# Optimization experiments

Measured on AMD Instinct MI355X. Metric: run time of the kernel, lower is better.

Reference implementation:

```python
import jax, jax.numpy as jnp
import numpy as np

M, K, N = 16, 8192, 8192
GROUP = 128


def setup_inputs() -> dict:
    key = jax.random.key(0)
    k1, k2, k3, k4 = jax.random.split(key, 4)
    x = jax.random.normal(k1, (M, K), dtype=jnp.float16)
    # packed INT4 weights: 8 nibbles per int32, row-major along K -> shape (K//8, N)
    qweight = jax.random.randint(k2, (K // 8, N), 0, 2147483647, dtype=jnp.int32)
    # per-group scales (K//GROUP, N); small positive values like real quant scales
    scales = (jax.random.uniform(k3, (K // GROUP, N), dtype=jnp.float16) * jnp.float16(0.01)
              + jnp.float16(0.001))
    bias = jax.random.normal(k4, (N,), dtype=jnp.float16) * jnp.float16(0.1)
    return {"x": x, "qweight": qweight, "scales": scales, "bias": bias}


def _dequant(qweight, scales):
    K8, n = qweight.shape
    shifts = jnp.arange(8, dtype=jnp.int32) * 4  # (8,)
    nib = (qweight[:, None, :] >> shifts[None, :, None]) & 0xF  # (K//8, 8, N)
    w = nib.reshape(K8 * 8, n).astype(scales.dtype) - jnp.asarray(8, scales.dtype)
    g = scales.shape[0]
    group = (K8 * 8) // g
    w = (w.reshape(g, group, n) * scales[:, None, :]).reshape(K8 * 8, n)
    return w  # (K, N) in scales dtype


def reference(x, qweight, scales, bias):
    # INT4 dequant (symmetric, zero-point 8) + GEMM + bias epilogue
    w = _dequant(qweight, scales)          # (K, N)
    out = jnp.dot(x, w) + bias             # (M, N)
    return out
```

## Files before the change

kernel.cpp:

```cpp
#include <hip/hip_runtime.h>


#define K_DIM 8192
#define N_DIM 8192

typedef _Float16 h2 __attribute__((ext_vector_type(2)));
typedef _Float16 h8 __attribute__((ext_vector_type(8)));
typedef float f32x4 __attribute__((ext_vector_type(4)));

union H8U { unsigned u[4]; h8 h; };

__device__ __forceinline__ unsigned pkrtz_u(float a, float b) {
  return __builtin_bit_cast(unsigned, __builtin_amdgcn_cvt_pkrtz(a, b));
}

__global__ __launch_bounds__(1024, 4) void qlin_kernel(
    const float* __restrict__ x,
    const int* __restrict__ qw,
    const float* __restrict__ scales,
    const float* __restrict__ bias,
    float* __restrict__ out) {
  __shared__ float red[16][512];

  const int tid = threadIdx.x;
  const int wave = tid >> 6;
  const int lane = tid & 63;
  const int c = lane & 15;
  const int quad = lane >> 4;
  const int nb = blockIdx.x * 32;

  f32x4 acc0 = {0.f, 0.f, 0.f, 0.f};
  f32x4 acc1 = {0.f, 0.f, 0.f, 0.f};

  const float* xp = x + (size_t)c * K_DIM + wave * 512 + quad * 8;
  const int* qp = qw + (size_t)(wave * 64 + quad) * N_DIM + nb + 2 * c;
  const float* sp = scales + (size_t)(wave * 4) * N_DIM + nb + 2 * c;

  const h2 koff = __builtin_bit_cast(h2, 0x64086408u);

#pragma unroll
  for (int g = 0; g < 4; ++g) {
    float2 sv = *(const float2*)sp;
    h2 s0 = __builtin_bit_cast(h2, pkrtz_u(sv.x, sv.x));
    h2 s1 = __builtin_bit_cast(h2, pkrtz_u(sv.y, sv.y));
#pragma unroll
    for (int it = 0; it < 4; ++it) {
      int2 q2 = *(const int2*)qp;
      float4 xa = *(const float4*)xp;
      float4 xb = *(const float4*)(xp + 4);
      H8U a, b0, b1;
      a.u[0] = pkrtz_u(xa.x, xb.x);
      a.u[1] = pkrtz_u(xa.y, xb.y);
      a.u[2] = pkrtz_u(xa.z, xb.z);
      a.u[3] = pkrtz_u(xa.w, xb.w);
      unsigned qa = (unsigned)q2.x, qb = (unsigned)q2.y;
#pragma unroll
      for (int p = 0; p < 4; ++p) {
        unsigned t0 = ((qa >> (4 * p)) & 0x000F000Fu) | 0x64006400u;
        unsigned t1 = ((qb >> (4 * p)) & 0x000F000Fu) | 0x64006400u;
        h2 w0 = (__builtin_bit_cast(h2, t0) - koff) * s0;
        h2 w1 = (__builtin_bit_cast(h2, t1) - koff) * s1;
        b0.u[p] = __builtin_bit_cast(unsigned, w0);
        b1.u[p] = __builtin_bit_cast(unsigned, w1);
      }
      acc0 = __builtin_amdgcn_mfma_f32_16x16x32_f16(a.h, b0.h, acc0, 0, 0, 0);
      acc1 = __builtin_amdgcn_mfma_f32_16x16x32_f16(a.h, b1.h, acc1, 0, 0, 0);
      qp += 4 * N_DIM;
      xp += 32;
    }
    sp += N_DIM;
  }

#pragma unroll
  for (int r = 0; r < 4; ++r) {
    int m = quad * 4 + r;
    red[wave][m * 32 + 2 * c] = acc0[r];
    red[wave][m * 32 + 2 * c + 1] = acc1[r];
  }
  __syncthreads();

  if (tid < 512) {
    int j = tid & 31;
    float v = 0.f;
#pragma unroll
    for (int w = 0; w < 16; ++w) v += red[w][tid];
    int n = nb + j;
    v += bias[n];
    out[(size_t)(tid >> 5) * N_DIM + n] = v;
  }
}

extern "C" void kernel_launch(void* const* d_in, const int* in_sizes, int n_in,
                              void* d_out, int out_size, void* d_ws, size_t ws_size,
                              hipStream_t stream) {
  const float* x      = (const float*)d_in[0];
  const int* qw       = (const int*)d_in[1];
  const float* scales = (const float*)d_in[2];
  const float* bias   = (const float*)d_in[3];
  float* out          = (float*)d_out;

  qlin_kernel<<<256, 1024, 0, stream>>>(x, qw, scales, bias, out);
}
```

Baseline: 93.00 us.

## Split-K with LDS-staged coalesced INT4 tiles and atomic accumulation

Replaces the one-block-per-32-columns kernel with a split-K grid of 512 blocks. Each block covers 256 columns by 512 K, stages packed INT4 weights into LDS with wide coalesced int4 loads, and reuses each activation fragment across four column tiles. Partial sums are reduced in LDS and then added to the output with float atomics. A separate kernel writes the bias into the output first. This aims to make weight loads coalesced and increase reuse, at the cost of an extra launch, atomic traffic, and non-deterministic summation order.

Result: slower. 94.92 us (+2.1%).

```diff
diff --git a/kernel.cpp b/kernel.cpp
--- a/kernel.cpp
+++ b/kernel.cpp
@@ -7,86 +7,109 @@
 typedef _Float16 h2 __attribute__((ext_vector_type(2)));
 typedef _Float16 h8 __attribute__((ext_vector_type(8)));
 typedef float f32x4 __attribute__((ext_vector_type(4)));
-
 union H8U { unsigned u[4]; h8 h; };
 
 __device__ __forceinline__ unsigned pkrtz_u(float a, float b) {
   return __builtin_bit_cast(unsigned, __builtin_amdgcn_cvt_pkrtz(a, b));
 }
 
-__global__ __launch_bounds__(1024, 4) void qlin_kernel(
+__global__ void bias_init_kernel(const float* __restrict__ bias, float* __restrict__ out) {
+  int i = blockIdx.x * 256 + threadIdx.x;
+  out[i] = bias[i & (N_DIM - 1)];
+}
+
+__global__ __launch_bounds__(512, 4) void qlin_main(
     const float* __restrict__ x,
     const int* __restrict__ qw,
     const float* __restrict__ scales,
-    const float* __restrict__ bias,
     float* __restrict__ out) {
-  __shared__ float red[16][512];
+  __shared__ int lds_q[16384];
 
   const int tid = threadIdx.x;
-  const int wave = tid >> 6;
-  const int lane = tid & 63;
-  const int c = lane & 15;
-  const int quad = lane >> 4;
-  const int nb = blockIdx.x * 32;
+  const int ntb = blockIdx.x & 31;
+  const int ksb = blockIdx.x >> 5;
+  const int nb = ntb << 8;
+  const int kb = ksb << 9;
+  const int rowbase = ksb << 6;
 
-  f32x4 acc0 = {0.f, 0.f, 0.f, 0.f};
-  f32x4 acc1 = {0.f, 0.f, 0.f, 0.f};
-
-  const float* xp = x + (size_t)c * K_DIM + wave * 512 + quad * 8;
-  const int* qp = qw + (size_t)(wave * 64 + quad) * N_DIM + nb + 2 * c;
-  const float* sp = scales + (size_t)(wave * 4) * N_DIM + nb + 2 * c;
-
-  const h2 koff = __builtin_bit_cast(h2, 0x64086408u);
-
+  const int* qg = qw + (size_t)rowbase * N_DIM + nb;
+  int4 v[8];
 #pragma unroll
-  for (int g = 0; g < 4; ++g) {
-    float2 sv = *(const float2*)sp;
-    h2 s0 = __builtin_bit_cast(h2, pkrtz_u(sv.x, sv.x));
-    h2 s1 = __builtin_bit_cast(h2, pkrtz_u(sv.y, sv.y));
+  for (int p = 0; p < 8; ++p) {
+    int idx = (p << 9) + tid;
+    int row = idx >> 6;
+    int c4 = (idx & 63) << 2;
+    v[p] = *(const int4*)(qg + (size_t)row * N_DIM + c4);
+  }
 #pragma unroll
-    for (int it = 0; it < 4; ++it) {
-      int2 q2 = *(const int2*)qp;
-      float4 xa = *(const float4*)xp;
-      float4 xb = *(const float4*)(xp + 4);
-      H8U a, b0, b1;
-      a.u[0] = pkrtz_u(xa.x, xb.x);
-      a.u[1] = pkrtz_u(xa.y, xb.y);
-      a.u[2] = pkrtz_u(xa.z, xb.z);
-      a.u[3] = pkrtz_u(xa.w, xb.w);
-      unsigned qa = (unsigned)q2.x, qb = (unsigned)q2.y;
-#pragma unroll
-      for (int p = 0; p < 4; ++p) {
-        unsigned t0 = ((qa >> (4 * p)) & 0x000F000Fu) | 0x64006400u;
-        unsigned t1 = ((qb >> (4 * p)) & 0x000F000Fu) | 0x64006400u;
-        h2 w0 = (__builtin_bit_cast(h2, t0) - koff) * s0;
-        h2 w1 = (__builtin_bit_cast(h2, t1) - koff) * s1;
-        b0.u[p] = __builtin_bit_cast(unsigned, w0);
-        b1.u[p] = __builtin_bit_cast(unsigned, w1);
-      }
-      acc0 = __builtin_amdgcn_mfma_f32_16x16x32_f16(a.h, b0.h, acc0, 0, 0, 0);
-      acc1 = __builtin_amdgcn_mfma_f32_16x16x32_f16(a.h, b1.h, acc1, 0, 0, 0);
-      qp += 4 * N_DIM;
-      xp += 32;
-    }
-    sp += N_DIM;
-  }
-
-#pragma unroll
-  for (int r = 0; r < 4; ++r) {
-    int m = quad * 4 + r;
-    red[wave][m * 32 + 2 * c] = acc0[r];
-    red[wave][m * 32 + 2 * c + 1] = acc1[r];
+  for (int p = 0; p < 8; ++p) {
+    int idx = (p << 9) + tid;
+    int row = idx >> 6;
+    int c4 = (idx & 63) << 2;
+    int L = (((row >> 2) << 4) + (c4 >> 4)) * 64 + ((row & 3) << 4) + (c4 & 15);
+    *(int4*)&lds_q[L] = v[p];
   }
   __syncthreads();
 
-  if (tid < 512) {
-    int j = tid & 31;
-    float v = 0.f;
+  const int wave = tid >> 6, lane = tid & 63;
+  const int wn = wave & 3, wk = wave >> 2;
+  const int c = lane & 15, q = lane >> 4;
+
+  h2 sc[2][4];
 #pragma unroll
-    for (int w = 0; w < 16; ++w) v += red[w][tid];
-    int n = nb + j;
-    v += bias[n];
-    out[(size_t)(tid >> 5) * N_DIM + n] = v;
+  for (int g2 = 0; g2 < 2; ++g2)
+#pragma unroll
+    for (int ct = 0; ct < 4; ++ct) {
+      float sv = scales[(size_t)((ksb << 2) + (wk << 1) + g2) * N_DIM +
+                        nb + (wn << 6) + (ct << 4) + c];
+      sc[g2][ct] = __builtin_bit_cast(h2, pkrtz_u(sv, sv));
+    }
+
+  const h2 koff = __builtin_bit_cast(h2, 0x64086408u);
+  f32x4 acc[4] = {{0.f,0.f,0.f,0.f},{0.f,0.f,0.f,0.f},{0.f,0.f,0.f,0.f},{0.f,0.f,0.f,0.f}};
+
+  const float* xp = x + (size_t)c * K_DIM + kb + (wk << 8) + (q << 3);
+#pragma unroll
+  for (int s = 0; s < 8; ++s) {
+    float4 xa = *(const float4*)xp;
+    float4 xb = *(const float4*)(xp + 4);
+    xp += 32;
+    H8U a;
+    a.u[0] = pkrtz_u(xa.x, xb.x);
+    a.u[1] = pkrtz_u(xa.y, xb.y);
+    a.u[2] = pkrtz_u(xa.z, xb.z);
+    a.u[3] = pkrtz_u(xa.w, xb.w);
+    int base = ((((wk << 3) + s) << 4) + (wn << 2)) * 64 + lane;
+#pragma unroll
+    for (int ct = 0; ct < 4; ++ct) {
+      unsigned qv = (unsigned)lds_q[base + (ct << 6)];
+      h2 s2 = sc[s >> 2][ct];
+      H8U b;
+#pragma unroll
+      for (int p = 0; p < 4; ++p) {
+        unsigned t = ((qv >> (4 * p)) & 0x000F000Fu) | 0x64006400u;
+        h2 w = (__builtin_bit_cast(h2, t) - koff) * s2;
+        b.u[p] = __builtin_bit_cast(unsigned, w);
+      }
+      acc[ct] = __builtin_amdgcn_mfma_f32_16x16x32_f16(a.h, b.h, acc[ct], 0, 0, 0);
+    }
+  }
+
+  __syncthreads();
+  float* red = (float*)lds_q;
+#pragma unroll
+  for (int ct = 0; ct < 4; ++ct)
+#pragma unroll
+    for (int r = 0; r < 4; ++r)
+      red[((wk << 4) + (q << 2) + r) * 256 + (wn << 6) + (ct << 4) + c] = acc[ct][r];
+  __syncthreads();
+
+#pragma unroll
+  for (int e = 0; e < 8; ++e) {
+    int idx = (e << 9) + tid;
+    int m = idx >> 8, j = idx & 255;
+    float vv = red[m * 256 + j] + red[(16 + m) * 256 + j];
+    unsafeAtomicAdd(&out[(size_t)m * N_DIM + nb + j], vv);
   }
 }
 
@@ -99,5 +122,6 @@
   const float* bias   = (const float*)d_in[3];
   float* out          = (float*)d_out;
 
-  qlin_kernel<<<256, 1024, 0, stream>>>(x, qw, scales, bias, out);
+  bias_init_kernel<<<512, 256, 0, stream>>>(bias, out);
+  qlin_main<<<512, 512, 0, stream>>>(x, qw, scales, out);
 }
```

## Split K across blocks with atomic reduction and prepack x to fp16

Applied to the files above, without the earlier changes.

The main kernel now splits K across four blocks per N tile (1024 blocks of 512 threads) and accumulates partial results into the output with atomic adds. The output is first initialised to the bias by a separate kernel. x is converted to packed fp16 MFMA layout once by a prepack kernel instead of in every block. All weight loads are issued up front and A-operand loads are double-buffered to expose more memory parallelism. The cost is two extra kernel launches, global atomics, and a non-deterministic summation order.

Result: faster. 86.12 us (-7.4%).

```diff
diff --git a/kernel.cpp b/kernel.cpp
--- a/kernel.cpp
+++ b/kernel.cpp
@@ -7,86 +7,107 @@
 typedef _Float16 h2 __attribute__((ext_vector_type(2)));
 typedef _Float16 h8 __attribute__((ext_vector_type(8)));
 typedef float f32x4 __attribute__((ext_vector_type(4)));
-
 union H8U { unsigned u[4]; h8 h; };
 
 __device__ __forceinline__ unsigned pkrtz_u(float a, float b) {
   return __builtin_bit_cast(unsigned, __builtin_amdgcn_cvt_pkrtz(a, b));
 }
+__device__ __forceinline__ h2 dup_h2(float v) {
+  return __builtin_bit_cast(h2, pkrtz_u(v, v));
+}
 
-__global__ __launch_bounds__(1024, 4) void qlin_kernel(
-    const float* __restrict__ x,
+__global__ void bias_init_kernel(const float* __restrict__ bias, float* __restrict__ out) {
+  int i = blockIdx.x * 256 + threadIdx.x;
+  out[i] = bias[i & (N_DIM - 1)];
+}
+
+__global__ void prepack_x_kernel(const float* __restrict__ x, unsigned* __restrict__ xpk) {
+  int S = blockIdx.x;
+  int L = threadIdx.x;
+  int q = L >> 4, m = L & 15;
+  const float* xp = x + (size_t)m * K_DIM + 32 * S + 8 * q;
+  float4 lo = *(const float4*)xp;
+  float4 hi = *(const float4*)(xp + 4);
+  unsigned* o = xpk + S * 256 + L * 4;
+  o[0] = pkrtz_u(lo.x, hi.x);
+  o[1] = pkrtz_u(lo.y, hi.y);
+  o[2] = pkrtz_u(lo.z, hi.z);
+  o[3] = pkrtz_u(lo.w, hi.w);
+}
+
+__global__ __launch_bounds__(512, 8) void qlin_main(
+    const unsigned* __restrict__ xpk,
     const int* __restrict__ qw,
     const float* __restrict__ scales,
-    const float* __restrict__ bias,
     float* __restrict__ out) {
-  __shared__ float red[16][512];
+  __shared__ float red[8][512];
 
   const int tid = threadIdx.x;
-  const int wave = tid >> 6;
+  const int wv = tid >> 6;
   const int lane = tid & 63;
   const int c = lane & 15;
   const int quad = lane >> 4;
-  const int nb = blockIdx.x * 32;
+  const int ntb = blockIdx.x & 255;
+  const int ksb = blockIdx.x >> 8;
+  const int nb = ntb * 32;
+  const int S0 = ksb * 64 + wv * 8;
+
+  const int* qp = qw + (size_t)(4 * S0 + quad) * N_DIM + nb + 2 * c;
+  int2 qv[8];
+#pragma unroll
+  for (int s = 0; s < 8; ++s) qv[s] = *(const int2*)(qp + (size_t)(4 * s) * N_DIM);
+  const float* sp = scales + (size_t)(S0 >> 2) * N_DIM + nb + 2 * c;
+  float2 svA = *(const float2*)sp;
+  float2 svB = *(const float2*)(sp + N_DIM);
+
+  const unsigned* ap = xpk + (size_t)S0 * 256 + lane * 4;
+  uint4 av[2];
+  av[0] = *(const uint4*)ap;
+
+  const h2 koff = __builtin_bit_cast(h2, 0x64086408u);
+  h2 s0A = dup_h2(svA.x), s1A = dup_h2(svA.y);
+  h2 s0B = dup_h2(svB.x), s1B = dup_h2(svB.y);
 
   f32x4 acc0 = {0.f, 0.f, 0.f, 0.f};
   f32x4 acc1 = {0.f, 0.f, 0.f, 0.f};
 
-  const float* xp = x + (size_t)c * K_DIM + wave * 512 + quad * 8;
-  const int* qp = qw + (size_t)(wave * 64 + quad) * N_DIM + nb + 2 * c;
-  const float* sp = scales + (size_t)(wave * 4) * N_DIM + nb + 2 * c;
-
-  const h2 koff = __builtin_bit_cast(h2, 0x64086408u);
-
 #pragma unroll
-  for (int g = 0; g < 4; ++g) {
-    float2 sv = *(const float2*)sp;
-    h2 s0 = __builtin_bit_cast(h2, pkrtz_u(sv.x, sv.x));
-    h2 s1 = __builtin_bit_cast(h2, pkrtz_u(sv.y, sv.y));
+  for (int s = 0; s < 8; ++s) {
+    if (s < 7) av[(s + 1) & 1] = *(const uint4*)(ap + (s + 1) * 256);
+    h2 s0 = (s < 4) ? s0A : s0B;
+    h2 s1 = (s < 4) ? s1A : s1B;
+    uint4 u = av[s & 1];
+    H8U a;
+    a.u[0] = u.x; a.u[1] = u.y; a.u[2] = u.z; a.u[3] = u.w;
+    unsigned qa = (unsigned)qv[s].x, qb = (unsigned)qv[s].y;
+    H8U b0, b1;
 #pragma unroll
-    for (int it = 0; it < 4; ++it) {
-      int2 q2 = *(const int2*)qp;
-      float4 xa = *(const float4*)xp;
-      float4 xb = *(const float4*)(xp + 4);
-      H8U a, b0, b1;
-      a.u[0] = pkrtz_u(xa.x, xb.x);
-      a.u[1] = pkrtz_u(xa.y, xb.y);
-      a.u[2] = pkrtz_u(xa.z, xb.z);
-      a.u[3] = pkrtz_u(xa.w, xb.w);
-      unsigned qa = (unsigned)q2.x, qb = (unsigned)q2.y;
-#pragma unroll
-      for (int p = 0; p < 4; ++p) {
-        unsigned t0 = ((qa >> (4 * p)) & 0x000F000Fu) | 0x64006400u;
-        unsigned t1 = ((qb >> (4 * p)) & 0x000F000Fu) | 0x64006400u;
-        h2 w0 = (__builtin_bit_cast(h2, t0) - koff) * s0;
-        h2 w1 = (__builtin_bit_cast(h2, t1) - koff) * s1;
-        b0.u[p] = __builtin_bit_cast(unsigned, w0);
-        b1.u[p] = __builtin_bit_cast(unsigned, w1);
-      }
-      acc0 = __builtin_amdgcn_mfma_f32_16x16x32_f16(a.h, b0.h, acc0, 0, 0, 0);
-      acc1 = __builtin_amdgcn_mfma_f32_16x16x32_f16(a.h, b1.h, acc1, 0, 0, 0);
-      qp += 4 * N_DIM;
-      xp += 32;
+    for (int p = 0; p < 4; ++p) {
+      unsigned t0 = ((qa >> (4 * p)) & 0x000F000Fu) | 0x64006400u;
+      unsigned t1 = ((qb >> (4 * p)) & 0x000F000Fu) | 0x64006400u;
+      h2 w0 = (__builtin_bit_cast(h2, t0) - koff) * s0;
+      h2 w1 = (__builtin_bit_cast(h2, t1) - koff) * s1;
+      b0.u[p] = __builtin_bit_cast(unsigned, w0);
+      b1.u[p] = __builtin_bit_cast(unsigned, w1);
     }
-    sp += N_DIM;
+    acc0 = __builtin_amdgcn_mfma_f32_16x16x32_f16(a.h, b0.h, acc0, 0, 0, 0);
+    acc1 = __builtin_amdgcn_mfma_f32_16x16x32_f16(a.h, b1.h, acc1, 0, 0, 0);
   }
 
 #pragma unroll
   for (int r = 0; r < 4; ++r) {
     int m = quad * 4 + r;
-    red[wave][m * 32 + 2 * c] = acc0[r];
-    red[wave][m * 32 + 2 * c + 1] = acc1[r];
+    red[wv][m * 32 + 2 * c] = acc0[r];
+    red[wv][m * 32 + 2 * c + 1] = acc1[r];
   }
   __syncthreads();
 
-  if (tid < 512) {
-    int j = tid & 31;
+  {
+    int j = tid & 31, m = tid >> 5;
     float v = 0.f;
 #pragma unroll
-    for (int w = 0; w < 16; ++w) v += red[w][tid];
-    int n = nb + j;
-    v += bias[n];
-    out[(size_t)(tid >> 5) * N_DIM + n] = v;
+    for (int w = 0; w < 8; ++w) v += red[w][tid];
+    unsafeAtomicAdd(&out[(size_t)m * N_DIM + nb + j], v);
   }
 }
 
@@ -98,6 +119,9 @@
   const float* scales = (const float*)d_in[2];
   const float* bias   = (const float*)d_in[3];
   float* out          = (float*)d_out;
+  unsigned* xpk       = (unsigned*)d_ws;
 
-  qlin_kernel<<<256, 1024, 0, stream>>>(x, qw, scales, bias, out);
+  bias_init_kernel<<<512, 256, 0, stream>>>(bias, out);
+  prepack_x_kernel<<<256, 64, 0, stream>>>(x, xpk);
+  qlin_main<<<1024, 512, 0, stream>>>(xpk, qw, scales, out);
 }
```
